# Kernel optimization log

Measured on AMD Instinct MI355X. Metric: run time of the kernel, lower is better.

The kernel has to match this reference:

```python
import jax, jax.numpy as jnp
import numpy as np


def setup_inputs() -> dict:
    key = jax.random.key(0)
    ks = jax.random.split(key, 7)
    B, S, D, R = 4, 4096, 1024, 16
    scale = 1.0 / np.sqrt(D)
    return {
        "x": jax.random.normal(ks[0], (B, S, D), dtype=jnp.float32),
        "W_qkv": jax.random.normal(ks[1], (3 * D, D), dtype=jnp.float32) * scale,
        "b_qkv": jax.random.normal(ks[2], (3 * D,), dtype=jnp.float32) * 0.02,
        "W_a_q": jax.random.normal(ks[3], (R, D), dtype=jnp.float32) * scale,
        "W_b_q": jnp.zeros((D, R), dtype=jnp.float32) + jax.random.normal(ks[4], (D, R), dtype=jnp.float32) * 0.02,
        "W_a_v": jax.random.normal(ks[5], (R, D), dtype=jnp.float32) * scale,
        "W_b_v": jax.random.normal(ks[6], (D, R), dtype=jnp.float32) * 0.02,
    }


def reference(x, W_qkv, b_qkv, W_a_q, W_b_q, W_a_v, W_b_v):
    D = W_a_q.shape[1]
    # base qkv projection: [B, S, 3D]
    qkv = jnp.einsum("bsd,ed->bse", x, W_qkv) + b_qkv
    # LoRA branches: x -> [B,S,r] -> [B,S,D]
    q_ba = jnp.einsum("bsr,dr->bsd", jnp.einsum("bsd,rd->bsr", x, W_a_q), W_b_q)
    v_ba = jnp.einsum("bsr,dr->bsd", jnp.einsum("bsd,rd->bsr", x, W_a_v), W_b_v)
    # add into q slice ([:D]) and v slice ([-D:])
    qkv = qkv.at[:, :, :D].add(q_ba)
    qkv = qkv.at[:, :, -D:].add(v_ba)
    return qkv
```

## Files before the change

### kernel.cpp

```cpp
#include <hip/hip_runtime.h>
#include <hip/hip_bf16.h>

typedef __bf16 bf16x4 __attribute__((ext_vector_type(4)));
typedef __bf16 bf16x8 __attribute__((ext_vector_type(8)));
typedef float floatx4 __attribute__((ext_vector_type(4)));

#define GLD16(gp, lp) __builtin_amdgcn_global_load_lds(                      \
    (const __attribute__((address_space(1))) void*)(gp),                     \
    (__attribute__((address_space(3))) void*)(lp), 16, 0, 0)

constexpr int Mdim = 16384;
constexpr int Ndim = 3072;
constexpr int Kdim = 1024;

static __device__ __forceinline__ bf16x8 cvt8(floatx4 lo, floatx4 hi) {
    bf16x8 r;
#pragma unroll
    for (int e = 0; e < 4; ++e) { r[e] = (__bf16)lo[e]; r[e + 4] = (__bf16)hi[e]; }
    return r;
}


__global__ __launch_bounds__(256) void build_weff(
    const float* __restrict__ Wqkv,
    const float* __restrict__ Waq,
    const float* __restrict__ Wbq,
    const float* __restrict__ Wav,
    const float* __restrict__ Wbv,
    __hip_bfloat16* __restrict__ Weff)
{
    const int idx = (blockIdx.x * 256 + threadIdx.x) * 4;
    const int e = idx >> 10;
    const int d = idx & 1023;
    floatx4 v = *(const floatx4*)(Wqkv + idx);
    if (e < 1024) {
#pragma unroll
        for (int r = 0; r < 16; ++r) {
            const float wb = Wbq[e * 16 + r];
            floatx4 wa = *(const floatx4*)(Waq + r * 1024 + d);
#pragma unroll
            for (int q = 0; q < 4; ++q) v[q] += wb * wa[q];
        }
    } else if (e >= 2048) {
        const int e2 = e - 2048;
#pragma unroll
        for (int r = 0; r < 16; ++r) {
            const float wb = Wbv[e2 * 16 + r];
            floatx4 wa = *(const floatx4*)(Wav + r * 1024 + d);
#pragma unroll
            for (int q = 0; q < 4; ++q) v[q] += wb * wa[q];
        }
    }
    bf16x4 o;
#pragma unroll
    for (int q = 0; q < 4; ++q) o[q] = (__bf16)v[q];
    *(bf16x4*)(Weff + idx) = o;
}

__global__ __launch_bounds__(256) void cvt_x(
    const float* __restrict__ x, __hip_bfloat16* __restrict__ xb)
{
    const size_t idx = ((size_t)blockIdx.x * 256 + threadIdx.x) * 8;
    bf16x8 r = cvt8(*(const floatx4*)(x + idx), *(const floatx4*)(x + idx + 4));
    *(bf16x8*)(xb + idx) = r;
}

__global__ __launch_bounds__(256, 2) void gemm_bf16_v3(
    const __hip_bfloat16* __restrict__ A,
    const __hip_bfloat16* __restrict__ Bw,
    const float* __restrict__ bias,
    float* __restrict__ C)
{
    constexpr int NT = Kdim / 64;
    __shared__ __hip_bfloat16 lds[2][2][128 * 64];

    const int t    = threadIdx.x;
    const int wave = t >> 6;
    const int lane = t & 63;
    const int wm   = wave >> 1;
    const int wn   = wave & 1;

    constexpr int NWG = (Mdim / 128) * (Ndim / 128);
    const int bid = (blockIdx.x & 7) * (NWG >> 3) + (blockIdx.x >> 3);
    const int bx  = bid % (Ndim / 128);
    const int by  = bid / (Ndim / 128);
    const int m0  = by * 128;
    const int n0  = bx * 128;

    const int srow0 = t >> 3;
    const int scb_s = ((t & 7) * 16) ^ ((srow0 & 7) << 4);

#define STAGE_TILE(nb_, kt_) do {                                              \
    const __hip_bfloat16* _ga = A  + (size_t)(m0 + srow0) * Kdim               \
                                + (kt_) * 64 + (scb_s >> 1);                   \
    const __hip_bfloat16* _gb = Bw + (size_t)(n0 + srow0) * Kdim               \
                                + (kt_) * 64 + (scb_s >> 1);                   \
    char* _la = (char*)&lds[nb_][0][0] + t * 16;                               \
    char* _lb = (char*)&lds[nb_][1][0] + t * 16;                               \
    GLD16(_ga,                      _la);                                      \
    GLD16(_ga + (size_t)32 * Kdim,  _la + 4096);                               \
    GLD16(_ga + (size_t)64 * Kdim,  _la + 8192);                               \
    GLD16(_ga + (size_t)96 * Kdim,  _la + 12288);                              \
    GLD16(_gb,                      _lb);                                      \
    GLD16(_gb + (size_t)32 * Kdim,  _lb + 4096);                               \
    GLD16(_gb + (size_t)64 * Kdim,  _lb + 8192);                               \
    GLD16(_gb + (size_t)96 * Kdim,  _lb + 12288);                              \
} while (0)

    const int fm   = lane & 15;
    const int fk2  = (lane >> 4) * 16;
    const int fxor = (fm & 7) << 4;
    const int cbs0 = fk2 ^ fxor;
    const int cbs1 = (64 + fk2) ^ fxor;

    floatx4 acc[4][4];
#pragma unroll
    for (int i = 0; i < 4; ++i)
#pragma unroll
        for (int j = 0; j < 4; ++j)
            acc[i][j] = (floatx4){0.f, 0.f, 0.f, 0.f};

    STAGE_TILE(0, 0);

    for (int kt = 0; kt < NT; ++kt) {
        const int nb = kt & 1;
        if (kt + 1 < NT) {
            STAGE_TILE(nb ^ 1, kt + 1);
            asm volatile("s_waitcnt vmcnt(8)" ::: "memory");
        } else {
            asm volatile("s_waitcnt vmcnt(0)" ::: "memory");
        }
        __builtin_amdgcn_s_barrier();

        const char* Ab = (const char*)&lds[nb][0][0];
        const char* Bb = (const char*)&lds[nb][1][0];
        bf16x8 aq[2][4], bq[2][4];
#pragma unroll
        for (int i = 0; i < 4; ++i) {
            aq[0][i] = *(const bf16x8*)(Ab + (wm * 64 + i * 16 + fm) * 128 + cbs0);
            aq[1][i] = *(const bf16x8*)(Ab + (wm * 64 + i * 16 + fm) * 128 + cbs1);
            bq[0][i] = *(const bf16x8*)(Bb + (wn * 64 + i * 16 + fm) * 128 + cbs0);
            bq[1][i] = *(const bf16x8*)(Bb + (wn * 64 + i * 16 + fm) * 128 + cbs1);
        }
        __builtin_amdgcn_s_setprio(1);
#pragma unroll
        for (int kk = 0; kk < 2; ++kk)
#pragma unroll
            for (int i = 0; i < 4; ++i)
#pragma unroll
                for (int j = 0; j < 4; ++j)
                    acc[i][j] = __builtin_amdgcn_mfma_f32_16x16x32_bf16(
                        aq[kk][i], bq[kk][j], acc[i][j], 0, 0, 0);
        __builtin_amdgcn_s_setprio(0);
        if (kt + 1 < NT)
            __builtin_amdgcn_s_barrier();
    }

    const int cn = lane & 15;
    const int cm = (lane >> 4) * 4;
    float bv[4];
#pragma unroll
    for (int j = 0; j < 4; ++j)
        bv[j] = bias[n0 + wn * 64 + j * 16 + cn];

#pragma unroll
    for (int i = 0; i < 4; ++i) {
        const int m = m0 + wm * 64 + i * 16 + cm;
#pragma unroll
        for (int j = 0; j < 4; ++j) {
            const int n = n0 + wn * 64 + j * 16 + cn;
            const size_t base = (size_t)m * Ndim + n;
#pragma unroll
            for (int r = 0; r < 4; ++r)
                C[base + (size_t)r * Ndim] = acc[i][j][r] + bv[j];
        }
    }
#undef STAGE_TILE
}


__global__ __launch_bounds__(256, 2) void gemm_bias_f32(
    const float* __restrict__ A, const float* __restrict__ Bw,
    const float* __restrict__ bias, float* __restrict__ C)
{
    constexpr int TK = 32;
    __shared__ __hip_bfloat16 As[128 * TK];
    __shared__ __hip_bfloat16 Bs[128 * TK];

    const int t    = threadIdx.x;
    const int wave = t >> 6;
    const int lane = t & 63;
    const int bx   = blockIdx.x % (Ndim / 128);
    const int by   = blockIdx.x / (Ndim / 128);
    const int m0   = by * 128;
    const int n0   = bx * 128;
    const int wm   = wave >> 1;
    const int wn   = wave & 1;
    const int srow = wave * 16 + (lane >> 2);
    const int scol = (lane & 3) * 8;

    const float* Ag0 = A  + (size_t)(m0 + srow) * Kdim + scol;
    const float* Ag1 = Ag0 + (size_t)64 * Kdim;
    const float* Bg0 = Bw + (size_t)(n0 + srow) * Kdim + scol;
    const float* Bg1 = Bg0 + (size_t)64 * Kdim;

    __hip_bfloat16* Al0 = &As[srow * TK + scol];
    __hip_bfloat16* Al1 = &As[(srow + 64) * TK + scol];
    __hip_bfloat16* Bl0 = &Bs[srow * TK + scol];
    __hip_bfloat16* Bl1 = &Bs[(srow + 64) * TK + scol];

    const int fm = lane & 15;
    const int fk = (lane >> 4) * 8;

    floatx4 acc[4][4];
#pragma unroll
    for (int i = 0; i < 4; ++i)
#pragma unroll
        for (int j = 0; j < 4; ++j)
            acc[i][j] = (floatx4){0.f, 0.f, 0.f, 0.f};

    for (int kt = 0; kt < Kdim; kt += TK) {
        bf16x8 a0 = cvt8(*(const floatx4*)(Ag0 + kt), *(const floatx4*)(Ag0 + kt + 4));
        bf16x8 a1 = cvt8(*(const floatx4*)(Ag1 + kt), *(const floatx4*)(Ag1 + kt + 4));
        bf16x8 b0 = cvt8(*(const floatx4*)(Bg0 + kt), *(const floatx4*)(Bg0 + kt + 4));
        bf16x8 b1 = cvt8(*(const floatx4*)(Bg1 + kt), *(const floatx4*)(Bg1 + kt + 4));
        __syncthreads();
        *(bf16x8*)Al0 = a0;
        *(bf16x8*)Al1 = a1;
        *(bf16x8*)Bl0 = b0;
        *(bf16x8*)Bl1 = b1;
        __syncthreads();

        bf16x8 af[4], bfr[4];
#pragma unroll
        for (int i = 0; i < 4; ++i) {
            af[i]  = *(const bf16x8*)&As[(wm * 64 + i * 16 + fm) * TK + fk];
            bfr[i] = *(const bf16x8*)&Bs[(wn * 64 + i * 16 + fm) * TK + fk];
        }
#pragma unroll
        for (int i = 0; i < 4; ++i)
#pragma unroll
            for (int j = 0; j < 4; ++j)
                acc[i][j] = __builtin_amdgcn_mfma_f32_16x16x32_bf16(af[i], bfr[j], acc[i][j], 0, 0, 0);
    }

    const int cn = lane & 15;
    const int cm = (lane >> 4) * 4;
    float bv[4];
#pragma unroll
    for (int j = 0; j < 4; ++j)
        bv[j] = bias[n0 + wn * 64 + j * 16 + cn];
#pragma unroll
    for (int i = 0; i < 4; ++i) {
        const int m = m0 + wm * 64 + i * 16 + cm;
#pragma unroll
        for (int j = 0; j < 4; ++j) {
            const int n = n0 + wn * 64 + j * 16 + cn;
            const size_t base = (size_t)m * Ndim + n;
#pragma unroll
            for (int r = 0; r < 4; ++r)
                C[base + (size_t)r * Ndim] = acc[i][j][r] + bv[j];
        }
    }
}

__global__ __launch_bounds__(256) void lora_rmw(
    const float* __restrict__ x,
    const float* __restrict__ Waq, const float* __restrict__ Wbq,
    const float* __restrict__ Wav, const float* __restrict__ Wbv,
    float* __restrict__ out)
{
    __shared__ float Pq[64][16];
    __shared__ float Pv[64][16];
    const int t  = threadIdx.x;
    const int m0 = blockIdx.x * 64;
    {
        const int row = t >> 2;
        const int r0  = (t & 3) * 4;
        float accq[4] = {0.f, 0.f, 0.f, 0.f};
        float accv[4] = {0.f, 0.f, 0.f, 0.f};
        const float* xr = x + (size_t)(m0 + row) * Kdim;
        for (int d = 0; d < Kdim; d += 4) {
            floatx4 xv = *(const floatx4*)(xr + d);
#pragma unroll
            for (int rr = 0; rr < 4; ++rr) {
                floatx4 wq = *(const floatx4*)(Waq + (size_t)(r0 + rr) * Kdim + d);
                floatx4 wv = *(const floatx4*)(Wav + (size_t)(r0 + rr) * Kdim + d);
#pragma unroll
                for (int e = 0; e < 4; ++e) {
                    accq[rr] += xv[e] * wq[e];
                    accv[rr] += xv[e] * wv[e];
                }
            }
        }
#pragma unroll
        for (int rr = 0; rr < 4; ++rr) {
            Pq[row][r0 + rr] = accq[rr];
            Pv[row][r0 + rr] = accv[rr];
        }
    }
    __syncthreads();
    const int col  = t * 8;
    const bool isq = col < 1024;
    const int nn0  = isq ? col : col - 1024;
    const int n    = isq ? col : col + 1024;
    const float* Wb = isq ? Wbq : Wbv;
    for (int row = 0; row < 64; ++row) {
        const float* P = isq ? Pq[row] : Pv[row];
        const size_t off = (size_t)(m0 + row) * Ndim + n;
        floatx4 o0 = *(const floatx4*)(out + off);
        floatx4 o1 = *(const floatx4*)(out + off + 4);
#pragma unroll
        for (int i = 0; i < 8; ++i) {
            floatx4 w0 = *(const floatx4*)(Wb + (size_t)(nn0 + i) * 16);
            floatx4 w1 = *(const floatx4*)(Wb + (size_t)(nn0 + i) * 16 + 4);
            floatx4 w2 = *(const floatx4*)(Wb + (size_t)(nn0 + i) * 16 + 8);
            floatx4 w3 = *(const floatx4*)(Wb + (size_t)(nn0 + i) * 16 + 12);
            float s = 0.f;
#pragma unroll
            for (int r = 0; r < 4; ++r)
                s += P[r] * w0[r] + P[r + 4] * w1[r] + P[r + 8] * w2[r] + P[r + 12] * w3[r];
            if (i < 4) o0[i] += s; else o1[i - 4] += s;
        }
        *(floatx4*)(out + off)     = o0;
        *(floatx4*)(out + off + 4) = o1;
    }
}

extern "C" void kernel_launch(void* const* d_in, const int* in_sizes, int n_in,
                              void* d_out, int out_size, void* d_ws, size_t ws_size,
                              hipStream_t stream)
{
    (void)in_sizes; (void)n_in; (void)out_size;
    const float* x    = (const float*)d_in[0];
    const float* Wqkv = (const float*)d_in[1];
    const float* bqkv = (const float*)d_in[2];
    const float* Waq  = (const float*)d_in[3];
    const float* Wbq  = (const float*)d_in[4];
    const float* Wav  = (const float*)d_in[5];
    const float* Wbv  = (const float*)d_in[6];
    float* out = (float*)d_out;

    const size_t WEFF_BYTES = (size_t)Ndim * Kdim * sizeof(__hip_bfloat16);
    const size_t XB_BYTES   = (size_t)Mdim * Kdim * sizeof(__hip_bfloat16);

    if (ws_size >= WEFF_BYTES + XB_BYTES) {
        __hip_bfloat16* Weff = (__hip_bfloat16*)d_ws;
        __hip_bfloat16* xb   = (__hip_bfloat16*)((char*)d_ws + WEFF_BYTES);
        build_weff<<<(Ndim * Kdim / 4) / 256, 256, 0, stream>>>(Wqkv, Waq, Wbq, Wav, Wbv, Weff);
        cvt_x<<<(int)(((size_t)Mdim * Kdim / 8) / 256), 256, 0, stream>>>(x, xb);
        gemm_bf16_v3<<<(Mdim / 128) * (Ndim / 128), 256, 0, stream>>>(xb, Weff, bqkv, out);
    } else {
        gemm_bias_f32<<<(Mdim / 128) * (Ndim / 128), 256, 0, stream>>>(x, Wqkv, bqkv, out);
        lora_rmw<<<Mdim / 64, 256, 0, stream>>>(x, Waq, Wbq, Wav, Wbv, out);
    }
}
```

Baseline: 372.9 us.

## Make GEMM persistent over six N tiles, overlapping epilogue stores with next tile

The bf16 GEMM now launches 512 workgroups, each walking six consecutive 128-wide N tiles for one M block. Staging of the next tile's first K-slice is prefetched across tile boundaries. The previous tile's biased accumulators are written with nontemporal stores interleaved into the first K iterations of the next tile, using hand-tuned vmcnt waits. This targets the epilogue store stall and launch/tail overhead. In exchange it doubles accumulator registers (accp), which could cause spills or lower occupancy, and the vmcnt counts are fragile.

New measurement: 435.0 us. 16.7% more time.

```diff
diff --git a/kernel.cpp b/kernel.cpp
--- a/kernel.cpp
+++ b/kernel.cpp
@@ -65,13 +65,14 @@
     *(bf16x8*)(xb + idx) = r;
 }
 
-__global__ __launch_bounds__(256, 2) void gemm_bf16_v3(
+__global__ __launch_bounds__(256, 2) void gemm_bf16_v4(
     const __hip_bfloat16* __restrict__ A,
     const __hip_bfloat16* __restrict__ Bw,
     const float* __restrict__ bias,
     float* __restrict__ C)
 {
-    constexpr int NT = Kdim / 64;
+    constexpr int NT  = Kdim / 64;
+    constexpr int TPB = 6;
     __shared__ __hip_bfloat16 lds[2][2][128 * 64];
 
     const int t    = threadIdx.x;
@@ -80,21 +81,18 @@
     const int wm   = wave >> 1;
     const int wn   = wave & 1;
 
-    constexpr int NWG = (Mdim / 128) * (Ndim / 128);
-    const int bid = (blockIdx.x & 7) * (NWG >> 3) + (blockIdx.x >> 3);
-    const int bx  = bid % (Ndim / 128);
-    const int by  = bid / (Ndim / 128);
-    const int m0  = by * 128;
-    const int n0  = bx * 128;
+    const int bid = (blockIdx.x & 7) * 64 + (blockIdx.x >> 3);
+    const int m0  = (bid >> 2) * 128;
+    const int ng  = (bid & 3) * TPB;
 
     const int srow0 = t >> 3;
     const int scb_s = ((t & 7) * 16) ^ ((srow0 & 7) << 4);
-
-#define STAGE_TILE(nb_, kt_) do {                                              \
-    const __hip_bfloat16* _ga = A  + (size_t)(m0 + srow0) * Kdim               \
-                                + (kt_) * 64 + (scb_s >> 1);                   \
-    const __hip_bfloat16* _gb = Bw + (size_t)(n0 + srow0) * Kdim               \
-                                + (kt_) * 64 + (scb_s >> 1);                   \
+    const __hip_bfloat16* Agb = A  + (size_t)(m0 + srow0) * Kdim + (scb_s >> 1);
+    const __hip_bfloat16* Bgb = Bw + (size_t)srow0 * Kdim + (scb_s >> 1);
+
+#define STAGE(Bg_, kt_, nb_) do {                                              \
+    const __hip_bfloat16* _ga = Agb + (kt_) * 64;                              \
+    const __hip_bfloat16* _gb = (Bg_) + (kt_) * 64;                            \
     char* _la = (char*)&lds[nb_][0][0] + t * 16;                               \
     char* _lb = (char*)&lds[nb_][1][0] + t * 16;                               \
     GLD16(_ga,                      _la);                                      \
@@ -112,70 +110,115 @@
     const int fxor = (fm & 7) << 4;
     const int cbs0 = fk2 ^ fxor;
     const int cbs1 = (64 + fk2) ^ fxor;
-
-    floatx4 acc[4][4];
+    const int cn   = lane & 15;
+    const int cm   = (lane >> 4) * 4;
+
+    floatx4 acc[4][4], accp[4][4];
 #pragma unroll
     for (int i = 0; i < 4; ++i)
 #pragma unroll
         for (int j = 0; j < 4; ++j)
             acc[i][j] = (floatx4){0.f, 0.f, 0.f, 0.f};
 
-    STAGE_TILE(0, 0);
-
-    for (int kt = 0; kt < NT; ++kt) {
-        const int nb = kt & 1;
-        if (kt + 1 < NT) {
-            STAGE_TILE(nb ^ 1, kt + 1);
-            asm volatile("s_waitcnt vmcnt(8)" ::: "memory");
-        } else {
-            asm volatile("s_waitcnt vmcnt(0)" ::: "memory");
-        }
-        __builtin_amdgcn_s_barrier();
-
-        const char* Ab = (const char*)&lds[nb][0][0];
-        const char* Bb = (const char*)&lds[nb][1][0];
-        bf16x8 aq[2][4], bq[2][4];
-#pragma unroll
-        for (int i = 0; i < 4; ++i) {
-            aq[0][i] = *(const bf16x8*)(Ab + (wm * 64 + i * 16 + fm) * 128 + cbs0);
-            aq[1][i] = *(const bf16x8*)(Ab + (wm * 64 + i * 16 + fm) * 128 + cbs1);
-            bq[0][i] = *(const bf16x8*)(Bb + (wn * 64 + i * 16 + fm) * 128 + cbs0);
-            bq[1][i] = *(const bf16x8*)(Bb + (wn * 64 + i * 16 + fm) * 128 + cbs1);
-        }
-        __builtin_amdgcn_s_setprio(1);
-#pragma unroll
-        for (int kk = 0; kk < 2; ++kk)
+    int n0  = ng * 128;
+    int n0p = n0;
+    float bv[4];
+    __builtin_amdgcn_sched_barrier(0);
+#pragma unroll
+    for (int j = 0; j < 4; ++j) bv[j] = bias[n0 + wn * 64 + j * 16 + cn];
+    __builtin_amdgcn_sched_barrier(0);
+
+    const __hip_bfloat16* Bg = Bgb + ((size_t)ng * 128) * Kdim;
+    STAGE(Bg, 0, 0);
+
+#pragma unroll 1
+    for (int tile = 0; tile < TPB; ++tile) {
+        const __hip_bfloat16* Bgn = Bg + (size_t)128 * Kdim;
+#pragma unroll
+        for (int kt = 0; kt < NT; ++kt) {
+            const int nb = kt & 1;
+            if (kt < NT - 1)           STAGE(Bg,  kt + 1, nb ^ 1);
+            else if (tile + 1 < TPB)   STAGE(Bgn, 0,      nb ^ 1);
+            if (tile > 0 && kt < 4) {
+#pragma unroll
+                for (int j = 0; j < 4; ++j) {
+                    const size_t base = (size_t)(m0 + wm * 64 + kt * 16 + cm) * Ndim
+                                      + (n0p + wn * 64 + j * 16 + cn);
+#pragma unroll
+                    for (int r = 0; r < 4; ++r)
+                        __builtin_nontemporal_store(accp[kt][j][r],
+                                                    &C[base + (size_t)r * Ndim]);
+                }
+            }
+            if (kt == NT - 1 && tile == TPB - 1)
+                asm volatile("s_waitcnt vmcnt(0)" ::: "memory");
+            else if (tile == 0)
+                asm volatile("s_waitcnt vmcnt(8)" ::: "memory");
+            else if (kt == 0)
+                asm volatile("s_waitcnt vmcnt(28)" ::: "memory");
+            else if (kt <= 3)
+                asm volatile("s_waitcnt vmcnt(40)" ::: "memory");
+            else if (kt == 4)
+                asm volatile("s_waitcnt vmcnt(24)" ::: "memory");
+            else
+                asm volatile("s_waitcnt vmcnt(8)" ::: "memory");
+            __builtin_amdgcn_s_barrier();
+
+            const char* Ab = (const char*)&lds[nb][0][0];
+            const char* Bb = (const char*)&lds[nb][1][0];
+            bf16x8 aq[2][4], bq[2][4];
+#pragma unroll
+            for (int i = 0; i < 4; ++i) {
+                aq[0][i] = *(const bf16x8*)(Ab + (wm * 64 + i * 16 + fm) * 128 + cbs0);
+                aq[1][i] = *(const bf16x8*)(Ab + (wm * 64 + i * 16 + fm) * 128 + cbs1);
+                bq[0][i] = *(const bf16x8*)(Bb + (wn * 64 + i * 16 + fm) * 128 + cbs0);
+                bq[1][i] = *(const bf16x8*)(Bb + (wn * 64 + i * 16 + fm) * 128 + cbs1);
+            }
+            __builtin_amdgcn_s_setprio(1);
+#pragma unroll
+            for (int kk = 0; kk < 2; ++kk)
+#pragma unroll
+                for (int i = 0; i < 4; ++i)
+#pragma unroll
+                    for (int j = 0; j < 4; ++j)
+                        acc[i][j] = __builtin_amdgcn_mfma_f32_16x16x32_bf16(
+                            aq[kk][i], bq[kk][j], acc[i][j], 0, 0, 0);
+            __builtin_amdgcn_s_setprio(0);
+            __builtin_amdgcn_s_barrier();
+        }
+        if (tile + 1 < TPB) {
 #pragma unroll
             for (int i = 0; i < 4; ++i)
 #pragma unroll
-                for (int j = 0; j < 4; ++j)
-                    acc[i][j] = __builtin_amdgcn_mfma_f32_16x16x32_bf16(
-                        aq[kk][i], bq[kk][j], acc[i][j], 0, 0, 0);
-        __builtin_amdgcn_s_setprio(0);
-        if (kt + 1 < NT)
-            __builtin_amdgcn_s_barrier();
-    }
-
-    const int cn = lane & 15;
-    const int cm = (lane >> 4) * 4;
-    float bv[4];
-#pragma unroll
-    for (int j = 0; j < 4; ++j)
-        bv[j] = bias[n0 + wn * 64 + j * 16 + cn];
+                for (int j = 0; j < 4; ++j) {
+#pragma unroll
+                    for (int r = 0; r < 4; ++r)
+                        accp[i][j][r] = acc[i][j][r] + bv[j];
+                    acc[i][j] = (floatx4){0.f, 0.f, 0.f, 0.f};
+                }
+            n0p = n0;
+            n0 += 128;
+            __builtin_amdgcn_sched_barrier(0);
+#pragma unroll
+            for (int j = 0; j < 4; ++j) bv[j] = bias[n0 + wn * 64 + j * 16 + cn];
+            __builtin_amdgcn_sched_barrier(0);
+            Bg = Bgn;
+        }
+    }
 
 #pragma unroll
     for (int i = 0; i < 4; ++i) {
         const int m = m0 + wm * 64 + i * 16 + cm;
 #pragma unroll
         for (int j = 0; j < 4; ++j) {
-            const int n = n0 + wn * 64 + j * 16 + cn;
-            const size_t base = (size_t)m * Ndim + n;
+            const size_t base = (size_t)m * Ndim + (n0 + wn * 64 + j * 16 + cn);
 #pragma unroll
             for (int r = 0; r < 4; ++r)
-                C[base + (size_t)r * Ndim] = acc[i][j][r] + bv[j];
-        }
-    }
-#undef STAGE_TILE
+                __builtin_nontemporal_store(acc[i][j][r] + bv[j],
+                                            &C[base + (size_t)r * Ndim]);
+        }
+    }
+#undef STAGE
 }
 
 
@@ -349,7 +392,7 @@
         __hip_bfloat16* xb   = (__hip_bfloat16*)((char*)d_ws + WEFF_BYTES);
         build_weff<<<(Ndim * Kdim / 4) / 256, 256, 0, stream>>>(Wqkv, Waq, Wbq, Wav, Wbv, Weff);
         cvt_x<<<(int)(((size_t)Mdim * Kdim / 8) / 256), 256, 0, stream>>>(x, xb);
-        gemm_bf16_v3<<<(Mdim / 128) * (Ndim / 128), 256, 0, stream>>>(xb, Weff, bqkv, out);
+        gemm_bf16_v4<<<512, 256, 0, stream>>>(xb, Weff, bqkv, out);
     } else {
         gemm_bias_f32<<<(Mdim / 128) * (Ndim / 128), 256, 0, stream>>>(x, Wqkv, bqkv, out);
         lora_rmw<<<Mdim / 64, 256, 0, stream>>>(x, Waq, Wbq, Wav, Wbv, out);
```
